# Kernel optimization log

Measured on AMD Instinct MI355X. Metric: run time of the kernel, lower is better.

The kernel has to match this reference:

```python
import jax, jax.numpy as jnp
import numpy as np


def _conv3d(x, w, stride, pad):
    return jax.lax.conv_general_dilated(
        x, w, window_strides=stride, padding=[(p, p) for p in pad],
        dimension_numbers=('NCDHW', 'OIDHW', 'NCDHW'))


def _bn(x, g, b, eps=1e-5):
    # BatchNorm3d in training mode: batch statistics over (N, D, H, W)
    m = x.mean((0, 2, 3, 4), keepdims=True)
    v = ((x - m) ** 2).mean((0, 2, 3, 4), keepdims=True)
    return (x - m) * jax.lax.rsqrt(v + eps) * g.reshape(1, -1, 1, 1, 1) + b.reshape(1, -1, 1, 1, 1)


def _lrelu(x):
    return jnp.where(x >= 0, x, 0.2 * x)


def _deform_conv3d(x, off, w, stride, pad, n_off_groups):
    # Deformable conv3d: offsets predict per-output-location (dz,dy,dx) shifts for
    # every kernel tap, shared across channel groups of size C//n_off_groups.
    B, C, D, H, W = x.shape
    O, _, kd, kh, kw = w.shape
    K = kd * kh * kw
    sd, sh, sw = stride
    pd, ph, pw = pad
    Do = (D + 2 * pd - kd) // sd + 1
    Ho = (H + 2 * ph - kh) // sh + 1
    Wo = (W + 2 * pw - kw) // sw + 1
    G = n_off_groups
    Cg = C // G
    # offset layout: [B, G, K, 3(dz,dy,dx), Do, Ho, Wo]
    off = off.reshape(B, G, K, 3, Do, Ho, Wo)
    kz, ky, kx = jnp.meshgrid(jnp.arange(kd), jnp.arange(kh), jnp.arange(kw), indexing='ij')
    bz = (jnp.arange(Do) * sd - pd).astype(x.dtype)[:, None, None]
    by = (jnp.arange(Ho) * sh - ph).astype(x.dtype)[None, :, None]
    bx = (jnp.arange(Wo) * sw - pw).astype(x.dtype)[None, None, :]
    kb = lambda a: a.reshape(-1).astype(x.dtype)[None, None, :, None, None, None]
    pz = off[:, :, :, 0] + bz + kb(kz)   # [B,G,K,Do,Ho,Wo]
    py = off[:, :, :, 1] + by + kb(ky)
    px = off[:, :, :, 2] + bx + kb(kx)
    z0, y0, x0 = jnp.floor(pz), jnp.floor(py), jnp.floor(px)
    fz, fy, fx = pz - z0, py - y0, px - x0
    xg = x.reshape(B, G, Cg, D * H * W)
    acc = jnp.zeros((B, G, Cg, K, Do, Ho, Wo), x.dtype)
    for cz in (0, 1):
        for cy in (0, 1):
            for cx in (0, 1):
                zc, yc, xc = z0 + cz, y0 + cy, x0 + cx
                wgt = ((fz if cz else 1 - fz) * (fy if cy else 1 - fy) * (fx if cx else 1 - fx))
                valid = ((zc >= 0) & (zc <= D - 1) & (yc >= 0) & (yc <= H - 1)
                         & (xc >= 0) & (xc <= W - 1)).astype(x.dtype)
                zi = jnp.clip(zc, 0, D - 1).astype(jnp.int32)
                yi = jnp.clip(yc, 0, H - 1).astype(jnp.int32)
                xi = jnp.clip(xc, 0, W - 1).astype(jnp.int32)
                idx = ((zi * H + yi) * W + xi).reshape(B, G, 1, -1)
                v = jnp.take_along_axis(xg, jnp.broadcast_to(idx, (B, G, Cg, idx.shape[-1])), axis=3)
                acc = acc + (wgt * valid)[:, :, None] * v.reshape(B, G, Cg, K, Do, Ho, Wo)
    val = acc.reshape(B, C, K, Do, Ho, Wo)
    return jnp.einsum('bckdhw,ock->bodhw', val, w.reshape(O, C, K))


def setup_inputs() -> dict:
    key = jax.random.key(0)
    ks = jax.random.split(key, 24)
    f32 = jnp.float32
    p = lambda k, shape, s=0.05: jax.random.normal(k, shape, f32) * s
    gb = lambda k, c: (1.0 + 0.05 * jax.random.normal(k, (c,), f32),
                       0.05 * jax.random.normal(jax.random.fold_in(k, 1), (c,), f32))
    g2, b2 = gb(ks[8], 64)
    g3, b3 = gb(ks[9], 128)
    g4, b4 = gb(ks[10], 256)
    g5, b5 = gb(ks[11], 512)
    g6, b6 = gb(ks[12], 512)
    return {
        'input': jax.random.normal(ks[0], (64, 3, 8, 128, 128), f32),
        'w1': p(ks[1], (32, 3, 4, 4, 4)),
        'w2': p(ks[2], (64, 32, 2, 4, 4)),
        'w3': p(ks[3], (128, 64, 2, 4, 4)),
        'w4': p(ks[4], (256, 128, 1, 4, 4)),
        'w_off': p(ks[5], (192, 256, 1, 4, 4), 0.01),
        'w5': p(ks[6], (512, 256, 1, 4, 4)),
        'w6': p(ks[7], (512, 512, 1, 4, 4)),
        'g2': g2, 'b2': b2, 'g3': g3, 'b3': b3, 'g4': g4, 'b4': b4,
        'g5': g5, 'b5': b5, 'g6': g6, 'b6': b6,
    }


def reference(input, w1, w2, w3, w4, w_off, w5, w6,
              g2, b2, g3, b3, g4, b4, g5, b5, g6, b6):
    encs = []
    out = _lrelu(_conv3d(input, w1, (2, 2, 2), (1, 1, 1)))          # norm_1 unused in forward
    encs.append(out)
    out = _lrelu(_bn(_conv3d(out, w2, (1, 2, 2), (0, 1, 1)), g2, b2))
    encs.append(out)
    out = _lrelu(_bn(_conv3d(out, w3, (1, 2, 2), (0, 1, 1)), g3, b3))
    encs.append(out)
    out = _lrelu(_bn(_conv3d(out, w4, (1, 2, 2), (0, 1, 1)), g4, b4))
    encs.append(out)
    off = _conv3d(out, w_off, (1, 2, 2), (0, 1, 1))
    out = _lrelu(_bn(_deform_conv3d(out, off, w5, (1, 2, 2), (0, 1, 1), 4), g5, b5))
    encs.append(out)
    out = _lrelu(_bn(_conv3d(out, w6, (1, 1, 1), (0, 0, 0)), g6, b6))
    encs.append(out)
    return tuple(encs)
```

## Files before the change

kernel.cpp:

```cpp
#include <hip/hip_runtime.h>
#include <hip/hip_bf16.h>
#include <cstdint>

typedef short bf16x8 __attribute__((ext_vector_type(8)));
typedef float f32x4 __attribute__((ext_vector_type(4)));

__device__ __forceinline__ float lrelu_f(float y) { return y >= 0.f ? y : 0.2f * y; }
__device__ __forceinline__ float b2f(unsigned short u) {
    union { unsigned int i; float f; } v; v.i = ((unsigned int)u) << 16; return v.f;
}
__device__ __forceinline__ unsigned short f2b(float f) {
    union { unsigned int i; float f; } v; v.f = f;
    unsigned int r = v.i + 0x7FFFu + ((v.i >> 16) & 1u);
    return (unsigned short)(r >> 16);
}

__global__ __launch_bounds__(256) void prep_k(
    const float* __restrict__ x, unsigned short* __restrict__ xc,
    const float* __restrict__ w1, const float* __restrict__ w2,
    const float* __restrict__ w3, const float* __restrict__ w4,
    const float* __restrict__ w_off, const float* __restrict__ w5,
    const float* __restrict__ w6, unsigned short* __restrict__ wp)
{
    int bid = blockIdx.x;
    if (bid < 131072) {
        int i = bid * 256 + threadIdx.x;
        int c = i & 3, w = (i >> 2) & 127, h = (i >> 9) & 127, d = (i >> 16) & 7, b = i >> 19;
        float v = (c < 3) ? x[(((size_t)b * 3 + c) * 8 + d) * 16384 + h * 128 + w] : 0.f;
        xc[i] = f2b(v);
        return;
    }
    long i = (long)(bid - 131072) * 256 + threadIdx.x;
    const float* src; int Cin, Tap, Cip; long rel;
    if (i < 8192)         { src = w1;    Cin = 3;   Tap = 64; Cip = 4;   rel = i; }
    else if (i < 73728)   { src = w2;    Cin = 32;  Tap = 32; Cip = 32;  rel = i - 8192; }
    else if (i < 335872)  { src = w3;    Cin = 64;  Tap = 32; Cip = 64;  rel = i - 73728; }
    else if (i < 860160)  { src = w4;    Cin = 128; Tap = 16; Cip = 128; rel = i - 335872; }
    else if (i < 1646592) { src = w_off; Cin = 256; Tap = 16; Cip = 256; rel = i - 860160; }
    else if (i < 3743744) { src = w5;    Cin = 256; Tap = 16; Cip = 256; rel = i - 1646592; }
    else                  { src = w6;    Cin = 512; Tap = 16; Cip = 512; rel = i - 3743744; }
    int c = (int)(rel % Cip);
    long t1 = rel / Cip;
    int t = (int)(t1 % Tap);
    long o = t1 / Tap;
    wp[i] = (c < Cin) ? f2b(src[((size_t)o * Cin + c) * Tap + t]) : (unsigned short)0;
}

template<int TM, int BN, int AMODE, int EPI>
__global__ __launch_bounds__(TM * 2) void igemm(
    const unsigned short* __restrict__ A, const unsigned short* __restrict__ Bw,
    void* __restrict__ Cout, float* __restrict__ sums,
    int M, int N, int K, int klen,
    int Ci, int Di, int Hi, int Wi,
    int kd, int kh, int kw,
    int sd, int sh_, int sw_, int pd, int ph_, int pw_,
    int Do, int Ho, int Wo)
{
    constexpr int NT = TM * 2;
    constexpr int NF = BN / 32;
    constexpr int WN = 16 * NF;
    constexpr int NBU = (BN * 4 + NT - 1) / NT;
    constexpr int NAU = (AMODE == 2) ? 4 : 2;
    constexpr int AH = 4 * TM * 8;
    constexpr int BH = 4 * BN * 8;
    __shared__ __align__(16) unsigned short As[2][4][TM][8];
    __shared__ __align__(16) unsigned short Bs[2][4][BN][8];
    __shared__ float redbuf[(EPI == 4) ? 2 * BN : 1];
    const int tid = threadIdx.x;
    const int m0 = blockIdx.x * TM;
    const int n0 = blockIdx.y * BN;
    const int k0 = blockIdx.z * klen;
    const int kend = min(K, k0 + klen);
    unsigned short* const As0 = &As[0][0][0][0];
    unsigned short* const Bs0 = &Bs[0][0][0][0];

    size_t bsrc[NBU];
    int boff[NBU];
#pragma unroll
    for (int i = 0; i < NBU; ++i) {
        int u = tid + i * NT;
        int row = u >> 2, s = u & 3;
        if (BN * 4 >= NT || u < BN * 4) {
            bsrc[i] = (size_t)(n0 + row) * K + s * 8;
            boff[i] = (s * BN + row) * 8;
        }
    }

    size_t asz[2];
    int asrc[NAU];
    unsigned long long amask[NAU];
    int aoff[NAU];

    if constexpr (AMODE == 0) {
#pragma unroll
        for (int i = 0; i < 2; ++i) {
            int u = tid + i * NT;
            int r = u >> 2, s = u & 3;
            asz[i] = (size_t)(m0 + r) * K + s * 8;
            aoff[i] = (s * TM + r) * 8;
        }
    } else {
#pragma unroll
        for (int i = 0; i < NAU; ++i) {
            int u = tid + i * NT;
            int r = (AMODE == 2) ? (u >> 3) : (u >> 2);
            int m = m0 + r;
            int ow = m % Wo; int t1 = m / Wo;
            int oh = t1 % Ho; t1 /= Ho;
            int od = t1 % Do; int b = t1 / Do;
            int id0 = od * sd - pd, ih0 = oh * sh_ - ph_, iw0 = ow * sw_ - pw_;
            unsigned long long xm = 0ull, yx = 0ull, mask = 0ull;
            for (int p = 0; p < kw; ++p) if ((unsigned)(iw0 + p) < (unsigned)Wi) xm |= 1ull << p;
            for (int p = 0; p < kh; ++p) if ((unsigned)(ih0 + p) < (unsigned)Hi) yx |= xm << (p * kw);
            for (int p = 0; p < kd; ++p) if ((unsigned)(id0 + p) < (unsigned)Di) mask |= yx << (p * kh * kw);
            amask[i] = mask;
            int bsp = ((b * Di + id0) * Hi + ih0) * Wi + iw0;
            if constexpr (AMODE == 1) {
                int s = u & 3;
                asrc[i] = bsp * Ci + s * 8;
                aoff[i] = (s * TM + r) * 8;
            } else {
                int j = u & 7;
                asrc[i] = (bsp + (j >> 2) * Wi + (j & 3)) * 4;
                aoff[i] = ((j >> 1) * TM + r) * 8 + (j & 1) * 4;
            }
        }
    }

    f32x4 acc[4][NF];
#pragma unroll
    for (int i = 0; i < 4; ++i)
#pragma unroll
        for (int j = 0; j < NF; ++j) acc[i][j] = (f32x4){0.f, 0.f, 0.f, 0.f};

    const int lane = tid & 63, wv = tid >> 6;
    const int wm = wv >> 1, wn = wv & 1;
    const int kg = lane >> 4, fr = lane & 15;

    int c0 = 0, kx = 0, ky = 0, tap = 0, doff = 0;
    if constexpr (AMODE == 1) {
        c0 = k0 % Ci;
        tap = k0 / Ci;
        kx = tap % kw;
        int t2 = tap / kw;
        ky = t2 % kh;
        int kz = t2 / kh;
        doff = (kz * Hi + ky) * Wi + kx;
    }
    auto advance = [&]() {
        c0 += 32;
        if (c0 >= Ci) {
            c0 = 0; ++tap; ++kx; ++doff;
            if (kx == kw) {
                kx = 0; doff += Wi - kw; ++ky;
                if (ky == kh) { ky = 0; doff += (Hi - kh) * Wi; }
            }
        }
    };

    for (int k = k0; k < kend; k += 64) {
#pragma unroll
        for (int i = 0; i < NBU; ++i)
            if (BN * 4 >= NT || tid + i * NT < BN * 4) {
                uint4 v0 = *(const uint4*)&Bw[bsrc[i] + k];
                uint4 v1 = *(const uint4*)&Bw[bsrc[i] + k + 32];
                *(uint4*)(Bs0 + boff[i]) = v0;
                *(uint4*)(Bs0 + BH + boff[i]) = v1;
            }
        if constexpr (AMODE == 0) {
#pragma unroll
            for (int i = 0; i < 2; ++i) {
                uint4 v0 = *(const uint4*)&A[asz[i] + k];
                uint4 v1 = *(const uint4*)&A[asz[i] + k + 32];
                *(uint4*)(As0 + aoff[i]) = v0;
                *(uint4*)(As0 + AH + aoff[i]) = v1;
            }
        } else if constexpr (AMODE == 1) {
            int t0 = tap, d0 = doff * Ci + c0;
            advance();
            int t1 = tap, d1 = doff * Ci + c0;
            advance();
#pragma unroll
            for (int i = 0; i < 2; ++i) {
                uint4 v0 = {0u, 0u, 0u, 0u}, v1 = {0u, 0u, 0u, 0u};
                if ((amask[i] >> t0) & 1ull) v0 = *(const uint4*)&A[(size_t)(asrc[i] + d0)];
                if ((amask[i] >> t1) & 1ull) v1 = *(const uint4*)&A[(size_t)(asrc[i] + d1)];
                *(uint4*)(As0 + aoff[i]) = v0;
                *(uint4*)(As0 + AH + aoff[i]) = v1;
            }
        } else {
            int kz = k >> 6;
            int U0 = kz * (Hi * Wi) * 4;
            int U1 = U0 + 2 * Wi * 4;
            int tap0 = k >> 2;
#pragma unroll
            for (int i = 0; i < 4; ++i) {
                int j = (tid + i * NT) & 7;
                uint2 v0 = {0u, 0u}, v1 = {0u, 0u};
                if ((amask[i] >> (tap0 + j)) & 1ull)
                    v0 = *(const uint2*)&A[(size_t)(asrc[i] + U0)];
                if ((amask[i] >> (tap0 + 8 + j)) & 1ull)
                    v1 = *(const uint2*)&A[(size_t)(asrc[i] + U1)];
                *(uint2*)(As0 + aoff[i]) = v0;
                *(uint2*)(As0 + AH + aoff[i]) = v1;
            }
        }
        __syncthreads();
#pragma unroll
        for (int kb = 0; kb < 2; ++kb) {
            bf16x8 af[4], bfr[NF];
#pragma unroll
            for (int mi = 0; mi < 4; ++mi)
                af[mi] = *(const bf16x8*)&As[kb][kg][wm * 64 + mi * 16 + fr][0];
#pragma unroll
            for (int ni = 0; ni < NF; ++ni)
                bfr[ni] = *(const bf16x8*)&Bs[kb][kg][wn * WN + ni * 16 + fr][0];
#pragma unroll
            for (int mi = 0; mi < 4; ++mi)
#pragma unroll
                for (int ni = 0; ni < NF; ++ni)
                    acc[mi][ni] = __builtin_amdgcn_mfma_f32_16x16x32_bf16(af[mi], bfr[ni], acc[mi][ni], 0, 0, 0);
        }
        __syncthreads();
    }

    if constexpr (EPI == 4) {
        for (int j = tid; j < 2 * BN; j += NT) redbuf[j] = 0.f;
        __syncthreads();
    }
    const int rb = m0 + wm * 64 + (lane >> 4) * 4;
    const int cb = n0 + wn * WN + fr;
    float p1[NF], p2[NF];
    if constexpr (EPI == 4) {
#pragma unroll
        for (int ni = 0; ni < NF; ++ni) { p1[ni] = 0.f; p2[ni] = 0.f; }
    }
#pragma unroll
    for (int mi = 0; mi < 4; ++mi)
#pragma unroll
        for (int rg = 0; rg < 4; ++rg) {
            size_t rowbase = (size_t)(rb + mi * 16 + rg) * N;
#pragma unroll
            for (int ni = 0; ni < NF; ++ni) {
                size_t idx = rowbase + cb + ni * 16;
                float vv = acc[mi][ni][rg];
                if constexpr (EPI == 0) ((unsigned short*)Cout)[idx] = f2b(vv);
                else if constexpr (EPI == 1) ((float*)Cout)[idx] = vv;
                else if constexpr (EPI == 2) atomicAdd((float*)Cout + idx, vv);
                else if constexpr (EPI == 3 || EPI == 5) ((unsigned short*)Cout)[idx] = f2b(lrelu_f(vv));
                else {
                    ((unsigned short*)Cout)[idx] = f2b(vv);
                    p1[ni] += vv; p2[ni] += vv * vv;
                }
            }
        }
    if constexpr (EPI == 4) {
#pragma unroll
        for (int ni = 0; ni < NF; ++ni) {
            int cl = wn * WN + ni * 16 + fr;
            atomicAdd(&redbuf[cl], p1[ni]);
            atomicAdd(&redbuf[BN + cl], p2[ni]);
        }
        __syncthreads();
        for (int j = tid; j < 2 * BN; j += NT) {
            int gcol = (j < BN) ? (n0 + j) : (N + n0 + j - BN);
            atomicAdd(&sums[gcol], redbuf[j]);
        }
    }
    if constexpr (EPI == 5) {
#pragma unroll
        for (int mi = 0; mi < 4; ++mi) {
            int mr = rb + mi * 16;
            int b = mr >> 14, ssp = mr & 16383;
            float4 f;
            f.x = lrelu_f(acc[mi][0][0]);
            f.y = lrelu_f(acc[mi][0][1]);
            f.z = lrelu_f(acc[mi][0][2]);
            f.w = lrelu_f(acc[mi][0][3]);
            *(float4*)&sums[((size_t)(b * 32 + cb)) * 16384 + ssp] = f;
        }
    }
}

__global__ __launch_bounds__(256) void f2b_sums(const float* __restrict__ in,
                                                unsigned short* __restrict__ o,
                                                float* __restrict__ sums,
                                                long totalSlots, int C)
{
    const int tid = threadIdx.x;
    long gid = (long)blockIdx.x * 256 + tid;
    long stride = (long)gridDim.x * 256;
    float s1[8], s2[8];
#pragma unroll
    for (int j = 0; j < 8; ++j) { s1[j] = 0.f; s2[j] = 0.f; }
    for (long s = gid; s < totalSlots; s += stride) {
        float4 a = *(const float4*)&in[s * 8];
        float4 b = *(const float4*)&in[s * 8 + 4];
        float f[8] = {a.x, a.y, a.z, a.w, b.x, b.y, b.z, b.w};
        unsigned short u[8];
#pragma unroll
        for (int j = 0; j < 8; ++j) { u[j] = f2b(f[j]); s1[j] += f[j]; s2[j] += f[j] * f[j]; }
        *(uint4*)&o[s * 8] = *(uint4*)u;
    }
    __shared__ float r1[2048], r2[2048];
#pragma unroll
    for (int j = 0; j < 8; ++j) { r1[tid * 8 + j] = s1[j]; r2[tid * 8 + j] = s2[j]; }
    __syncthreads();
    int G = C >> 3;
    for (int c = tid; c < C; c += 256) {
        int grp = c >> 3, j = c & 7;
        float a = 0.f, b = 0.f;
        for (int th = grp; th < 256; th += G) { a += r1[th * 8 + j]; b += r2[th * 8 + j]; }
        atomicAdd(&sums[c], a);
        atomicAdd(&sums[C + c], b);
    }
}

__global__ __launch_bounds__(256) void bn_fin(float* __restrict__ sums,
                                              const float* __restrict__ g, const float* __restrict__ bt,
                                              float* __restrict__ sc, float* __restrict__ sh,
                                              int C, float invcnt)
{
    int c = blockIdx.x * 256 + threadIdx.x;
    if (c >= C) return;
    float mean = sums[c] * invcnt;
    float var = sums[C + c] * invcnt - mean * mean;
    float rs = rsqrtf(var + 1e-5f);
    float scl = g[c] * rs;
    sc[c] = scl;
    sh[c] = bt[c] - mean * scl;
    sums[c] = 0.f;
    sums[C + c] = 0.f;
}

__global__ __launch_bounds__(256) void bn_apply_t(
    unsigned short* __restrict__ x, const float* __restrict__ sc, const float* __restrict__ sh,
    float* __restrict__ outN, int C, int TC, int S)
{
    __shared__ __align__(16) float T[64][68];
    const int tid = threadIdx.x;
    const long m0 = (long)blockIdx.x * 64;
    const int c0 = blockIdx.y * TC;
    const int spr = TC >> 3;
    const int lg = (spr == 8) ? 3 : 2;
    const int tot = 64 * spr;
    for (int u = tid; u < tot; u += 256) {
        int r = u >> lg, sl = u & (spr - 1);
        size_t idx = (size_t)(m0 + r) * C + c0 + sl * 8;
        uint4 v = *(uint4*)&x[idx];
        unsigned short* pv = (unsigned short*)&v;
#pragma unroll
        for (int j = 0; j < 8; ++j) {
            int c = c0 + sl * 8 + j;
            float f = b2f(pv[j]);
            f = lrelu_f(f * sc[c] + sh[c]);
            pv[j] = f2b(f);
            T[sl * 8 + j][r] = f;
        }
        *(uint4*)&x[idx] = v;
    }
    __syncthreads();
    const int tpc = 256 / TC;
    const int rpt = 64 / tpc;
    int cl = tid / tpc;
    int r0 = (tid % tpc) * rpt;
    int c = c0 + cl;
    if ((S & 63) == 0) {
        long b = m0 / S;
        long s0 = m0 - b * S;
        float* op = outN + ((size_t)b * C + c) * S + s0 + r0;
        for (int r = 0; r < rpt; r += 4)
            *(float4*)(op + r) = *(float4*)&T[cl][r0 + r];
    } else {
        for (int r = 0; r < rpt; ++r) {
            long m = m0 + r0 + r;
            long b = m / S, s = m - b * S;
            outN[((size_t)b * C + c) * S + s] = T[cl][r0 + r];
        }
    }
}

__global__ __launch_bounds__(256) void deform_val(
    const unsigned short* __restrict__ xcl, const float* __restrict__ offc,
    unsigned short* __restrict__ val)
{
    int bs = blockIdx.x;
    int b = bs >> 5, s = bs & 31;
    int od = s >> 4, oh = (s >> 2) & 3, ow = s & 3;
    __shared__ float cw[64][8];
    __shared__ int cidx[64][8];
    int tid = threadIdx.x;
    if (tid < 64) {
        int gk = tid, k = gk & 15;
        int ky = k >> 2, kx = k & 3;
        const float* op = offc + (size_t)bs * 192 + gk * 3;
        float pz = op[0] + (float)od;
        float py = op[1] + (float)(oh * 2 - 1 + ky);
        float px = op[2] + (float)(ow * 2 - 1 + kx);
        float z0 = floorf(pz), y0 = floorf(py), x0 = floorf(px);
        float fz = pz - z0, fy = py - y0, fx = px - x0;
#pragma unroll
        for (int ci = 0; ci < 8; ++ci) {
            int cz = ci >> 2, cy = (ci >> 1) & 1, cx = ci & 1;
            float zc = z0 + cz, yc = y0 + cy, xc = x0 + cx;
            bool ok = zc >= 0.f && zc <= 1.f && yc >= 0.f && yc <= 7.f && xc >= 0.f && xc <= 7.f;
            int zi = min(max((int)zc, 0), 1);
            int yi = min(max((int)yc, 0), 7);
            int xi = min(max((int)xc, 0), 7);
            float wz = cz ? fz : 1.f - fz;
            float wy = cy ? fy : 1.f - fy;
            float wx = cx ? fx : 1.f - fx;
            cw[gk][ci] = ok ? wz * wy * wx : 0.f;
            cidx[gk][ci] = (zi * 8 + yi) * 8 + xi;
        }
    }
    __syncthreads();
    const unsigned short* xb = xcl + (size_t)b * 128 * 256;
    unsigned short* vo = val + (size_t)bs * 4096;
    for (int j = tid; j < 4096; j += 256) {
        int c = j & 255, tap = j >> 8;
        int gk = ((c >> 6) << 4) | tap;
        float v = 0.f;
#pragma unroll
        for (int i = 0; i < 8; ++i)
            v += cw[gk][i] * b2f(xb[(size_t)cidx[gk][i] * 256 + c]);
        vo[j] = f2b(v);
    }
}

extern "C" void kernel_launch(void* const* d_in, const int* in_sizes, int n_in,
                              void* d_out, int out_size, void* d_ws, size_t ws_size,
                              hipStream_t stream)
{
    (void)in_sizes; (void)n_in; (void)out_size; (void)ws_size;
    const float* x     = (const float*)d_in[0];
    const float* w1    = (const float*)d_in[1];
    const float* w2    = (const float*)d_in[2];
    const float* w3    = (const float*)d_in[3];
    const float* w4    = (const float*)d_in[4];
    const float* w_off = (const float*)d_in[5];
    const float* w5    = (const float*)d_in[6];
    const float* w6    = (const float*)d_in[7];
    const float* g2 = (const float*)d_in[8];  const float* b2 = (const float*)d_in[9];
    const float* g3 = (const float*)d_in[10]; const float* b3 = (const float*)d_in[11];
    const float* g4 = (const float*)d_in[12]; const float* b4 = (const float*)d_in[13];
    const float* g5 = (const float*)d_in[14]; const float* b5 = (const float*)d_in[15];
    const float* g6 = (const float*)d_in[16]; const float* b6 = (const float*)d_in[17];

    float* out = (float*)d_out;
    float* enc0 = out;
    float* enc1 = out + 33554432;
    float* enc2 = out + 46137344;
    float* enc3 = out + 50331648;
    float* enc4 = out + 52428800;
    float* enc5 = out + 53477376;

    char* W = (char*)d_ws;
    unsigned short* wpk  = (unsigned short*)(W + 0);
    unsigned short* w1p  = (unsigned short*)(W + 0);
    unsigned short* w2p  = (unsigned short*)(W + 16384);
    unsigned short* w3p  = (unsigned short*)(W + 147456);
    unsigned short* w4p  = (unsigned short*)(W + 671744);
    unsigned short* wofp = (unsigned short*)(W + 1720320);
    unsigned short* w5p  = (unsigned short*)(W + 3293184);
    unsigned short* w6p  = (unsigned short*)(W + 7487488);
    float* sums          = (float*)(W + 15876096);
    float* sc            = (float*)(W + 15880192);
    float* sh            = (float*)(W + 15882240);
    float* offc          = (float*)(W + 15884288);
    unsigned short* xcl  = (unsigned short*)(W + 17457152);
    unsigned short* e1c  = (unsigned short*)(W + 17457152);
    unsigned short* e2c  = (unsigned short*)(W + 42622976);
    unsigned short* e3c  = (unsigned short*)(W + 51011584);
    unsigned short* e0c  = (unsigned short*)(W + 84566016);
    unsigned short* valb = (unsigned short*)(W + 84566016);
    float* raw5          = (float*)(W + 101343232);
    unsigned short* e4c  = (unsigned short*)(W + 105537536);
    float* raw6          = (float*)(W + 107634688);
    unsigned short* e5c  = (unsigned short*)(W + 107896832);

    hipMemsetAsync(sums, 0, 4096, stream);
    prep_k<<<162080, 256, 0, stream>>>(x, xcl, w1, w2, w3, w4, w_off, w5, w6, wpk);

    igemm<256, 32, 2, 5><<<dim3(4096, 1, 1), 512, 0, stream>>>(
        xcl, w1p, e0c, enc0, 1048576, 32, 256, 256,
        4, 8, 128, 128, 4, 4, 4, 2, 2, 2, 1, 1, 1, 4, 64, 64);

    igemm<256, 64, 1, 4><<<dim3(768, 1, 1), 512, 0, stream>>>(
        e0c, w2p, e1c, sums, 196608, 64, 1024, 1024,
        32, 4, 64, 64, 2, 4, 4, 1, 2, 2, 0, 1, 1, 3, 32, 32);
    bn_fin<<<1, 256, 0, stream>>>(sums, g2, b2, sc, sh, 64, 1.f / 196608.f);
    bn_apply_t<<<dim3(3072, 1), 256, 0, stream>>>(e1c, sc, sh, enc1, 64, 64, 3072);

    igemm<256, 64, 1, 4><<<dim3(128, 2), 512, 0, stream>>>(
        e1c, w3p, e2c, sums, 32768, 128, 2048, 2048,
        64, 3, 32, 32, 2, 4, 4, 1, 2, 2, 0, 1, 1, 2, 16, 16);
    bn_fin<<<1, 256, 0, stream>>>(sums, g3, b3, sc, sh, 128, 1.f / 32768.f);
    bn_apply_t<<<dim3(512, 2), 256, 0, stream>>>(e2c, sc, sh, enc2, 128, 64, 512);

    igemm<128, 64, 1, 4><<<dim3(64, 4), 256, 0, stream>>>(
        e2c, w4p, e3c, sums, 8192, 256, 2048, 2048,
        128, 2, 16, 16, 1, 4, 4, 1, 2, 2, 0, 1, 1, 2, 8, 8);
    bn_fin<<<1, 256, 0, stream>>>(sums, g4, b4, sc, sh, 256, 1.f / 8192.f);
    bn_apply_t<<<dim3(128, 4), 256, 0, stream>>>(e3c, sc, sh, enc3, 256, 64, 128);

    hipMemsetAsync(offc, 0, 1572864, stream);
    igemm<128, 64, 1, 2><<<dim3(16, 3, 8), 256, 0, stream>>>(
        e3c, wofp, offc, nullptr, 2048, 192, 4096, 512,
        256, 2, 8, 8, 1, 4, 4, 1, 2, 2, 0, 1, 1, 2, 4, 4);

    deform_val<<<2048, 256, 0, stream>>>(e3c, offc, valb);
    hipMemsetAsync(raw5, 0, 4194304, stream);
    igemm<128, 64, 0, 2><<<dim3(16, 8, 8), 256, 0, stream>>>(
        valb, w5p, raw5, nullptr, 2048, 512, 4096, 512,
        0, 0, 0, 0, 1, 1, 1, 1, 1, 1, 0, 0, 0, 1, 1, 1);
    f2b_sums<<<256, 256, 0, stream>>>(raw5, e4c, sums, 131072L, 512);
    bn_fin<<<2, 256, 0, stream>>>(sums, g5, b5, sc, sh, 512, 1.f / 2048.f);
    bn_apply_t<<<dim3(32, 8), 256, 0, stream>>>(e4c, sc, sh, enc4, 512, 64, 32);

    hipMemsetAsync(raw6, 0, 262144, stream);
    igemm<128, 64, 0, 2><<<dim3(1, 8, 32), 256, 0, stream>>>(
        e4c, w6p, raw6, nullptr, 128, 512, 8192, 256,
        0, 0, 0, 0, 1, 1, 1, 1, 1, 1, 0, 0, 0, 1, 1, 1);
    f2b_sums<<<32, 256, 0, stream>>>(raw6, e5c, sums, 8192L, 512);
    bn_fin<<<2, 256, 0, stream>>>(sums, g6, b6, sc, sh, 512, 1.f / 128.f);
    bn_apply_t<<<dim3(2, 8), 256, 0, stream>>>(e5c, sc, sh, enc5, 512, 64, 2);
}
```

Measured before the change: 538.0 us.

## Fold BN finalize into apply, merge memsets, and remap GEMM block order

Removes the separate bn_fin kernels. Each bn_apply_t block now computes per-channel scale and shift from the accumulated sums into shared memory. Each BN layer gets its own sums slice, so none has to be zeroed between layers, and all zero-initialised scratch buffers (offsets, raw5, raw6, sums) are placed together and cleared with one memset. The igemm kernel also permutes blockIdx.x in groups of 8 when the grid is divisible by 8, likely to spread adjacent M tiles across XCDs or improve cache locality. The intent is to cut launch count and small-kernel overhead, at the cost of recomputing the BN finalize redundantly in every apply block.

```diff
diff --git a/kernel.cpp b/kernel.cpp
--- a/kernel.cpp
+++ b/kernel.cpp
@@ -67,7 +67,10 @@
     __shared__ __align__(16) unsigned short Bs[2][4][BN][8];
     __shared__ float redbuf[(EPI == 4) ? 2 * BN : 1];
     const int tid = threadIdx.x;
-    const int m0 = blockIdx.x * TM;
+    int bx = blockIdx.x;
+    if ((gridDim.x & 7) == 0)
+        bx = (bx & 7) * (gridDim.x >> 3) + (bx >> 3);
+    const int m0 = bx * TM;
     const int n0 = blockIdx.y * BN;
     const int k0 = blockIdx.z * klen;
     const int kend = min(K, k0 + klen);
@@ -316,31 +319,26 @@
     }
 }
 
-__global__ __launch_bounds__(256) void bn_fin(float* __restrict__ sums,
-                                              const float* __restrict__ g, const float* __restrict__ bt,
-                                              float* __restrict__ sc, float* __restrict__ sh,
-                                              int C, float invcnt)
-{
-    int c = blockIdx.x * 256 + threadIdx.x;
-    if (c >= C) return;
-    float mean = sums[c] * invcnt;
-    float var = sums[C + c] * invcnt - mean * mean;
-    float rs = rsqrtf(var + 1e-5f);
-    float scl = g[c] * rs;
-    sc[c] = scl;
-    sh[c] = bt[c] - mean * scl;
-    sums[c] = 0.f;
-    sums[C + c] = 0.f;
-}
-
 __global__ __launch_bounds__(256) void bn_apply_t(
-    unsigned short* __restrict__ x, const float* __restrict__ sc, const float* __restrict__ sh,
-    float* __restrict__ outN, int C, int TC, int S)
+    unsigned short* __restrict__ x, const float* __restrict__ sums,
+    const float* __restrict__ g, const float* __restrict__ bt,
+    float* __restrict__ outN, int C, int TC, int S, float invcnt)
 {
     __shared__ __align__(16) float T[64][68];
+    __shared__ float scs[64], shs[64];
     const int tid = threadIdx.x;
     const long m0 = (long)blockIdx.x * 64;
     const int c0 = blockIdx.y * TC;
+    if (tid < TC) {
+        int c = c0 + tid;
+        float mean = sums[c] * invcnt;
+        float var = sums[C + c] * invcnt - mean * mean;
+        float rs = rsqrtf(var + 1e-5f);
+        float scl = g[c] * rs;
+        scs[tid] = scl;
+        shs[tid] = bt[c] - mean * scl;
+    }
+    __syncthreads();
     const int spr = TC >> 3;
     const int lg = (spr == 8) ? 3 : 2;
     const int tot = 64 * spr;
@@ -351,11 +349,11 @@
         unsigned short* pv = (unsigned short*)&v;
 #pragma unroll
         for (int j = 0; j < 8; ++j) {
-            int c = c0 + sl * 8 + j;
+            int cl = sl * 8 + j;
             float f = b2f(pv[j]);
-            f = lrelu_f(f * sc[c] + sh[c]);
+            f = lrelu_f(f * scs[cl] + shs[cl]);
             pv[j] = f2b(f);
-            T[sl * 8 + j][r] = f;
+            T[cl][r] = f;
         }
         *(uint4*)&x[idx] = v;
     }
@@ -464,22 +462,25 @@
     unsigned short* wofp = (unsigned short*)(W + 1720320);
     unsigned short* w5p  = (unsigned short*)(W + 3293184);
     unsigned short* w6p  = (unsigned short*)(W + 7487488);
-    float* sums          = (float*)(W + 15876096);
-    float* sc            = (float*)(W + 15880192);
-    float* sh            = (float*)(W + 15882240);
-    float* offc          = (float*)(W + 15884288);
     unsigned short* xcl  = (unsigned short*)(W + 17457152);
     unsigned short* e1c  = (unsigned short*)(W + 17457152);
     unsigned short* e2c  = (unsigned short*)(W + 42622976);
     unsigned short* e3c  = (unsigned short*)(W + 51011584);
     unsigned short* e0c  = (unsigned short*)(W + 84566016);
     unsigned short* valb = (unsigned short*)(W + 84566016);
-    float* raw5          = (float*)(W + 101343232);
     unsigned short* e4c  = (unsigned short*)(W + 105537536);
-    float* raw6          = (float*)(W + 107634688);
     unsigned short* e5c  = (unsigned short*)(W + 107896832);
-
-    hipMemsetAsync(sums, 0, 4096, stream);
+    char* Z = W + 151674880;
+    float* offc = (float*)(Z);
+    float* raw5 = (float*)(Z + 1572864);
+    float* raw6 = (float*)(Z + 5767168);
+    float* sums = (float*)(Z + 6029312);
+    float* sums2 = sums + 1024;
+    float* sums3 = sums + 2048;
+    float* sums4 = sums + 3072;
+    float* sums5 = sums + 4096;
+
+    hipMemsetAsync(Z, 0, 6053888, stream);
     prep_k<<<162080, 256, 0, stream>>>(x, xcl, w1, w2, w3, w4, w_off, w5, w6, wpk);
 
     igemm<256, 32, 2, 5><<<dim3(4096, 1, 1), 512, 0, stream>>>(
@@ -489,40 +490,32 @@
     igemm<256, 64, 1, 4><<<dim3(768, 1, 1), 512, 0, stream>>>(
         e0c, w2p, e1c, sums, 196608, 64, 1024, 1024,
         32, 4, 64, 64, 2, 4, 4, 1, 2, 2, 0, 1, 1, 3, 32, 32);
-    bn_fin<<<1, 256, 0, stream>>>(sums, g2, b2, sc, sh, 64, 1.f / 196608.f);
-    bn_apply_t<<<dim3(3072, 1), 256, 0, stream>>>(e1c, sc, sh, enc1, 64, 64, 3072);
+    bn_apply_t<<<dim3(3072, 1), 256, 0, stream>>>(e1c, sums, g2, b2, enc1, 64, 64, 3072, 1.f / 196608.f);
 
     igemm<256, 64, 1, 4><<<dim3(128, 2), 512, 0, stream>>>(
-        e1c, w3p, e2c, sums, 32768, 128, 2048, 2048,
+        e1c, w3p, e2c, sums2, 32768, 128, 2048, 2048,
         64, 3, 32, 32, 2, 4, 4, 1, 2, 2, 0, 1, 1, 2, 16, 16);
-    bn_fin<<<1, 256, 0, stream>>>(sums, g3, b3, sc, sh, 128, 1.f / 32768.f);
-    bn_apply_t<<<dim3(512, 2), 256, 0, stream>>>(e2c, sc, sh, enc2, 128, 64, 512);
+    bn_apply_t<<<dim3(512, 2), 256, 0, stream>>>(e2c, sums2, g3, b3, enc2, 128, 64, 512, 1.f / 32768.f);
 
     igemm<128, 64, 1, 4><<<dim3(64, 4), 256, 0, stream>>>(
-        e2c, w4p, e3c, sums, 8192, 256, 2048, 2048,
+        e2c, w4p, e3c, sums3, 8192, 256, 2048, 2048,
         128, 2, 16, 16, 1, 4, 4, 1, 2, 2, 0, 1, 1, 2, 8, 8);
-    bn_fin<<<1, 256, 0, stream>>>(sums, g4, b4, sc, sh, 256, 1.f / 8192.f);
-    bn_apply_t<<<dim3(128, 4), 256, 0, stream>>>(e3c, sc, sh, enc3, 256, 64, 128);
-
-    hipMemsetAsync(offc, 0, 1572864, stream);
+    bn_apply_t<<<dim3(128, 4), 256, 0, stream>>>(e3c, sums3, g4, b4, enc3, 256, 64, 128, 1.f / 8192.f);
+
     igemm<128, 64, 1, 2><<<dim3(16, 3, 8), 256, 0, stream>>>(
         e3c, wofp, offc, nullptr, 2048, 192, 4096, 512,
         256, 2, 8, 8, 1, 4, 4, 1, 2, 2, 0, 1, 1, 2, 4, 4);
 
     deform_val<<<2048, 256, 0, stream>>>(e3c, offc, valb);
-    hipMemsetAsync(raw5, 0, 4194304, stream);
     igemm<128, 64, 0, 2><<<dim3(16, 8, 8), 256, 0, stream>>>(
         valb, w5p, raw5, nullptr, 2048, 512, 4096, 512,
         0, 0, 0, 0, 1, 1, 1, 1, 1, 1, 0, 0, 0, 1, 1, 1);
-    f2b_sums<<<256, 256, 0, stream>>>(raw5, e4c, sums, 131072L, 512);
-    bn_fin<<<2, 256, 0, stream>>>(sums, g5, b5, sc, sh, 512, 1.f / 2048.f);
-    bn_apply_t<<<dim3(32, 8), 256, 0, stream>>>(e4c, sc, sh, enc4, 512, 64, 32);
-
-    hipMemsetAsync(raw6, 0, 262144, stream);
+    f2b_sums<<<256, 256, 0, stream>>>(raw5, e4c, sums4, 131072L, 512);
+    bn_apply_t<<<dim3(32, 8), 256, 0, stream>>>(e4c, sums4, g5, b5, enc4, 512, 64, 32, 1.f / 2048.f);
+
     igemm<128, 64, 0, 2><<<dim3(1, 8, 32), 256, 0, stream>>>(
         e4c, w6p, raw6, nullptr, 128, 512, 8192, 256,
         0, 0, 0, 0, 1, 1, 1, 1, 1, 1, 0, 0, 0, 1, 1, 1);
-    f2b_sums<<<32, 256, 0, stream>>>(raw6, e5c, sums, 8192L, 512);
-    bn_fin<<<2, 256, 0, stream>>>(sums, g6, b6, sc, sh, 512, 1.f / 128.f);
-    bn_apply_t<<<dim3(2, 8), 256, 0, stream>>>(e5c, sc, sh, enc5, 512, 64, 2);
-}
+    f2b_sums<<<32, 256, 0, stream>>>(raw6, e5c, sums5, 8192L, 512);
+    bn_apply_t<<<dim3(2, 8), 256, 0, stream>>>(e5c, sums5, g6, b6, enc5, 512, 64, 2, 1.f / 128.f);
+}
```

Result: no change. 544.8 us (+1.3%).
